# Performance work log

Measured on AMD Instinct MI355X. Metric: run time of the kernel, lower is better.

Reference implementation:

```python
import jax, jax.numpy as jnp
import numpy as np

LEAKY_SLOPE = 0.2  # PyG GATv2Conv default negative_slope


def gatv2_layer(x, src, dst, Wl, Wr, att, bias, concat):
    """PyG GATv2Conv (eval mode, dropout off, self-loops already in src/dst).
    x: [N, Din]; Wl/Wr: [Din, H*C]; att: [H, C]; bias: [H*C] or [C].
    """
    N = x.shape[0]
    H, C = att.shape
    xl = (x @ Wl).reshape(N, H, C)   # source transform
    xr = (x @ Wr).reshape(N, H, C)   # target transform
    # per-edge GATv2 score: att . leakyrelu(x_l[j] + x_r[i])
    e = jax.nn.leaky_relu(xl[src] + xr[dst], negative_slope=LEAKY_SLOPE)  # [E, H, C]
    score = jnp.einsum('ehc,hc->eh', e, att)                              # [E, H]
    # segment softmax over incoming edges of each dst node
    m = jax.ops.segment_max(score, dst, num_segments=N)                   # [N, H]
    a = jnp.exp(score - m[dst])
    denom = jax.ops.segment_sum(a, dst, num_segments=N)                   # [N, H]
    alpha = a / denom[dst]                                                # [E, H]
    out = jax.ops.segment_sum(xl[src] * alpha[..., None], dst, num_segments=N)  # [N, H, C]
    out = out.reshape(N, H * C) if concat else out.mean(axis=1)
    return out + bias


def setup_inputs() -> dict:
    key = jax.random.key(0)
    ks = jax.random.split(key, 10)
    N, D, E = 20000, 128, 320000
    HID, HEADS, OUT = 64, 8, 32
    x = jax.random.normal(ks[0], (N, D), dtype=jnp.float32)
    edge_index = jax.random.randint(ks[1], (2, E), 0, N)
    glorot = lambda k, shape, fan: jax.random.normal(k, shape, jnp.float32) * (1.0 / np.sqrt(fan))
    W1l = glorot(ks[2], (D, HEADS * HID), D)
    W1r = glorot(ks[3], (D, HEADS * HID), D)
    att1 = glorot(ks[4], (HEADS, HID), HID)
    b1 = jnp.zeros((HEADS * HID,), jnp.float32)
    W2l = glorot(ks[5], (HEADS * HID, 64), HEADS * HID)
    W2r = glorot(ks[6], (HEADS * HID, 64), HEADS * HID)
    att2 = glorot(ks[7], (1, 64), 64)
    b2 = jnp.zeros((64,), jnp.float32)
    Wlin = glorot(ks[8], (64, OUT), 64)
    blin = jnp.zeros((OUT,), jnp.float32)
    return {"x": x, "edge_index": edge_index, "W1l": W1l, "W1r": W1r, "att1": att1,
            "b1": b1, "W2l": W2l, "W2r": W2r, "att2": att2, "b2": b2,
            "Wlin": Wlin, "blin": blin}


def reference(x, edge_index, W1l, W1r, att1, b1, W2l, W2r, att2, b2, Wlin, blin):
    N = x.shape[0]
    loop = jnp.arange(N)
    src = jnp.concatenate([edge_index[0], loop])  # PyG add_self_loops=True
    dst = jnp.concatenate([edge_index[1], loop])
    h = jax.nn.elu(gatv2_layer(x, src, dst, W1l, W1r, att1, b1, concat=True))
    h = jax.nn.elu(gatv2_layer(h, src, dst, W2l, W2r, att2, b2, concat=False))
    return jax.nn.elu(h @ Wlin + blin)
```

## Files before the change

### kernel.cpp

```cpp
#include <hip/hip_runtime.h>
#include <hip/hip_bf16.h>

typedef __attribute__((ext_vector_type(8))) short short8;
typedef __attribute__((ext_vector_type(4))) short short4v;
typedef __attribute__((ext_vector_type(4))) float floatx4;
typedef __attribute__((ext_vector_type(2))) float float2v;
typedef __attribute__((ext_vector_type(4))) int int4v;
typedef __attribute__((ext_vector_type(2))) int int2v;

#define LOG2E 1.44269504f

__device__ __forceinline__ short f2b(float f) {
    __hip_bfloat16 hb = __float2bfloat16(f);
    unsigned short us; __builtin_memcpy(&us, &hb, 2);
    return (short)us;
}
__device__ __forceinline__ float2v bpair(int p) {
    unsigned ulo = ((unsigned)p) << 16;
    unsigned uhi = ((unsigned)p) & 0xFFFF0000u;
    float flo, fhi;
    __builtin_memcpy(&flo, &ulo, 4);
    __builtin_memcpy(&fhi, &uhi, 4);
    float2v r; r.x = flo; r.y = fhi; return r;
}

__device__ __forceinline__ float2v pk_add(float2v a, float2v b) {
    float2v d;
    asm("v_pk_add_f32 %0, %1, %2" : "=v"(d) : "v"(a), "v"(b));
    return d;
}
__device__ __forceinline__ float2v pk_fma(float2v a, float2v b, float2v c) {
    float2v d;
    asm("v_pk_fma_f32 %0, %1, %2, %3" : "=v"(d) : "v"(a), "v"(b), "v"(c));
    return d;
}
__device__ __forceinline__ float2v pk_abs(float2v a) {
    float2v d;
    d.x = __builtin_fabsf(a.x);
    d.y = __builtin_fabsf(a.y);
    return d;
}

template<int CTRL>
__device__ __forceinline__ float dppadd(float x) {
    int xi; __builtin_memcpy(&xi, &x, 4);
    int yi = __builtin_amdgcn_update_dpp(0, xi, CTRL, 0xF, 0xF, false);
    float y; __builtin_memcpy(&y, &yi, 4);
    return x + y;
}
__device__ __forceinline__ float red8(float x) {
    x = dppadd<0xB1>(x);
    x = dppadd<0x4E>(x);
    x = dppadd<0x141>(x);
    return x;
}
__device__ __forceinline__ float red16(float x) {
    return dppadd<0x140>(red8(x));
}

__global__ void prep_all(const float* __restrict__ x,
                         const float* __restrict__ W1l, const float* __restrict__ W1r,
                         const float* __restrict__ W2l, const float* __restrict__ W2r,
                         short* __restrict__ xb, short* __restrict__ w1t,
                         short* __restrict__ w2t, int nx4,
                         const int* __restrict__ esrc, const int* __restrict__ edst,
                         int E, int N, int* __restrict__ counts,
                         unsigned short* __restrict__ srcs) {
    int tid = blockIdx.x * blockDim.x + threadIdx.x;
    int ET = E + N;
    if (tid < ET) {
        int d, s;
        if (tid < E) { d = edst[tid]; s = esrc[tid]; }
        else { d = tid - E; s = d; }
        int pos = atomicAdd(&counts[d], 1);
        if (pos < 64) srcs[(d << 6) + pos] = (unsigned short)s;
    }
    int idx = tid;
    if (idx < nx4) {
        floatx4 v = *(const floatx4*)(x + idx * 4);
        short4v o; o[0] = f2b(v[0]); o[1] = f2b(v[1]); o[2] = f2b(v[2]); o[3] = f2b(v[3]);
        *(short4v*)(xb + idx * 4) = o;
        return;
    }
    idx -= nx4;
    if (idx < 131072) {
        int n = idx >> 7, k = idx & 127;
        float v = (n < 512) ? W1l[k * 512 + n] : W1r[k * 512 + (n - 512)];
        w1t[idx] = f2b(v);
        return;
    }
    idx -= 131072;
    if (idx < 65536) {
        int n = idx >> 9, k = idx & 511;
        float v = (n < 64) ? W2l[k * 64 + n] : W2r[k * 64 + (n - 64)];
        w2t[idx] = f2b(v);
    }
}

__global__ __launch_bounds__(256) void gemm1(const short* __restrict__ A,
                                             const short* __restrict__ Bt,
                                             short* __restrict__ xl1, short* __restrict__ xr1,
                                             int M) {
    __shared__ short As[64 * 136];
    __shared__ short Bs[128 * 136];
    int t = threadIdx.x;
    int w = t >> 6, L = t & 63, q = L >> 4, s = L & 15;
    int p = blockIdx.x + (blockIdx.y << 3);
    int my = gridDim.y;
    int ww = (p & 7) * my + (p >> 3);
    int M0 = (ww >> 3) * 64, N0 = (ww & 7) * 128;
    #pragma unroll
    for (int i = 0; i < 4; ++i) {
        int c = t + i * 256;
        int r = c >> 4, col = (c & 15) * 8;
        int gr = M0 + r;
        short8 v = {};
        if (gr < M) v = *(const short8*)(A + (size_t)gr * 128 + col);
        *(short8*)(&As[r * 136 + col]) = v;
    }
    #pragma unroll
    for (int i = 0; i < 8; ++i) {
        int c = t + i * 256;
        int r = c >> 4, col = (c & 15) * 8;
        short8 v = *(const short8*)(Bt + (size_t)(N0 + r) * 128 + col);
        *(short8*)(&Bs[r * 136 + col]) = v;
    }
    __syncthreads();
    short8 a[4];
    #pragma unroll
    for (int kk = 0; kk < 4; ++kk)
        a[kk] = *(const short8*)(&As[(w * 16 + s) * 136 + kk * 32 + q * 8]);
    floatx4 acc[8] = {};
    #pragma unroll
    for (int tt = 0; tt < 8; ++tt) {
        #pragma unroll
        for (int kk = 0; kk < 4; ++kk) {
            short8 b = *(const short8*)(&Bs[(tt * 16 + s) * 136 + kk * 32 + q * 8]);
            acc[tt] = __builtin_amdgcn_mfma_f32_16x16x32_bf16(a[kk], b, acc[tt], 0, 0, 0);
        }
    }
    __syncthreads();
    #pragma unroll
    for (int tt = 0; tt < 8; ++tt) {
        #pragma unroll
        for (int rg = 0; rg < 4; ++rg) {
            int rl = w * 16 + q * 4 + rg;
            As[rl * 136 + tt * 16 + s] = f2b(acc[tt][rg]);
        }
    }
    __syncthreads();
    short* Cb = (N0 < 512) ? xl1 : xr1;
    int cb = (N0 < 512) ? N0 : N0 - 512;
    size_t M64 = (size_t)M * 64;
    #pragma unroll
    for (int i = 0; i < 4; ++i) {
        int c = t + i * 256;
        int r = c >> 4, col = (c & 15) * 8;
        int row = M0 + r;
        if (row < M) {
            short8 v = *(const short8*)(&As[r * 136 + col]);
            int cc = cb + col;
            *(short8*)(Cb + (size_t)(cc >> 6) * M64 + (size_t)row * 64 + (cc & 63)) = v;
        }
    }
}

__global__ __launch_bounds__(256) void gemm2(const short* __restrict__ A,
                                             const short* __restrict__ Bt,
                                             short* __restrict__ C, int M) {
    __shared__ short As[32 * 72];
    __shared__ short Bs[64 * 72];
    int t = threadIdx.x;
    int w = t >> 6, L = t & 63, q = L >> 4, s = L & 15;
    int rw = (w >> 1) * 16, cw = (w & 1) * 32;
    int p = blockIdx.x + gridDim.x * blockIdx.y;
    int nwg = gridDim.x * 2;
    int qq = nwg >> 3, rr = nwg & 7;
    int kx = p & 7, tx = p >> 3;
    int ww = (kx < rr ? kx * (qq + 1) : rr * (qq + 1) + (kx - rr) * qq) + tx;
    int M0 = (ww >> 1) * 32, N0 = (ww & 1) * 64;
    size_t M64 = (size_t)M * 64;
    floatx4 acc[2] = {};
    for (int k0 = 0; k0 < 512; k0 += 64) {
        {
            int r = t >> 3, col = (t & 7) * 8;
            int gr = M0 + r;
            short8 v = {};
            if (gr < M) v = *(const short8*)(A + (size_t)(k0 >> 6) * M64 + (size_t)gr * 64 + col);
            *(short8*)(&As[r * 72 + col]) = v;
        }
        #pragma unroll
        for (int i = 0; i < 2; ++i) {
            int c = t + i * 256;
            int r = c >> 3, col = (c & 7) * 8;
            short8 v = *(const short8*)(Bt + (size_t)(N0 + r) * 512 + k0 + col);
            *(short8*)(&Bs[r * 72 + col]) = v;
        }
        __syncthreads();
        #pragma unroll
        for (int kk = 0; kk < 2; ++kk) {
            short8 a = *(const short8*)(&As[(rw + s) * 72 + kk * 32 + q * 8]);
            #pragma unroll
            for (int tt = 0; tt < 2; ++tt) {
                short8 b = *(const short8*)(&Bs[(cw + tt * 16 + s) * 72 + kk * 32 + q * 8]);
                acc[tt] = __builtin_amdgcn_mfma_f32_16x16x32_bf16(a, b, acc[tt], 0, 0, 0);
            }
        }
        __syncthreads();
    }
    #pragma unroll
    for (int tt = 0; tt < 2; ++tt) {
        #pragma unroll
        for (int rg = 0; rg < 4; ++rg) {
            int rl = rw + q * 4 + rg;
            As[rl * 72 + cw + tt * 16 + s] = f2b(acc[tt][rg]);
        }
    }
    __syncthreads();
    {
        int r = t >> 3, col = (t & 7) * 8;
        int row = M0 + r;
        if (row < M) {
            short8 v = *(const short8*)(&As[r * 72 + col]);
            *(short8*)(C + (size_t)row * 128 + N0 + col) = v;
        }
    }
}

__global__ __launch_bounds__(256) void gat_l1(const short* __restrict__ xlh,
                       const short* __restrict__ xrh,
                       const int* __restrict__ counts,
                       const unsigned short* __restrict__ srcs,
                       const float* __restrict__ att, const float* __restrict__ bias,
                       short* __restrict__ h1h, int Nn) {
    int bid = blockIdx.x;
    int h = bid & 7, nb = bid >> 3;
    int t = threadIdx.x;
    int w = t >> 6, L = t & 63;
    int i = nb * 4 + w;
    if (i >= Nn) return;
    int g = L >> 3;
    int o8 = (L & 7) * 8;
    size_t slice = (size_t)h * ((size_t)Nn * 64);
    const short* Bh = xlh + slice;
    float2v xrv[4], at6[4], at4[4];
    {
        float av[8];
        *(floatx4*)av       = *(const floatx4*)(att + h * 64 + o8);
        *(floatx4*)(av + 4) = *(const floatx4*)(att + h * 64 + o8 + 4);
        int4v x4 = *(const int4v*)(xrh + slice + (size_t)i * 64 + o8);
        #pragma unroll
        for (int c = 0; c < 4; ++c) {
            xrv[c] = bpair(x4[c]);
            at6[c].x = av[2 * c]     * (0.6f * LOG2E);
            at6[c].y = av[2 * c + 1] * (0.6f * LOG2E);
            at4[c].x = av[2 * c]     * (0.4f * LOG2E);
            at4[c].y = av[2 * c + 1] * (0.4f * LOG2E);
        }
    }
    int jv = srcs[(i << 6) + L];
    int deg = counts[i]; deg = deg > 64 ? 64 : deg;
    float2v acc[4] = {};
    float dnm = 0.f;

    auto fetchj = [&](int e) -> int {
        int idx = e + g;
        idx = idx < deg ? idx : 0;
        return __shfl(jv, idx, 64);
    };
    auto ldrow = [&](int j) -> int4v {
        return *(const int4v*)(Bh + (((unsigned)j) << 6) + o8);
    };
    auto process = [&](int4v a4, int e) {
        float2v v[4]; float2v pp = {};
        #pragma unroll
        for (int c = 0; c < 4; ++c) {
            v[c] = bpair(a4[c]);
            float2v tv = pk_add(v[c], xrv[c]);
            pp = pk_fma(at6[c], tv, pp);
            pp = pk_fma(at4[c], pk_abs(tv), pp);
        }
        float e2 = __builtin_amdgcn_exp2f(red8(pp.x + pp.y));
        e2 = (e + g < deg) ? e2 : 0.f;
        dnm += e2;
        float2v ev; ev.x = e2; ev.y = e2;
        #pragma unroll
        for (int c = 0; c < 4; ++c)
            acc[c] = pk_fma(ev, v[c], acc[c]);
    };

    int4v cur = ldrow(fetchj(0));
    int e = 0;
    for (; e + 8 < deg; e += 8) {
        int4v nxt = ldrow(fetchj(e + 8));
        process(cur, e);
        cur = nxt;
    }
    process(cur, e);

    dnm += __shfl_xor(dnm, 8, 64);
    dnm += __shfl_xor(dnm, 16, 64);
    dnm += __shfl_xor(dnm, 32, 64);
    #pragma unroll
    for (int c = 0; c < 4; ++c) {
        acc[c].x += __shfl_xor(acc[c].x, 8, 64);
        acc[c].x += __shfl_xor(acc[c].x, 16, 64);
        acc[c].x += __shfl_xor(acc[c].x, 32, 64);
        acc[c].y += __shfl_xor(acc[c].y, 8, 64);
        acc[c].y += __shfl_xor(acc[c].y, 16, 64);
        acc[c].y += __shfl_xor(acc[c].y, 32, 64);
    }
    if (g == 0) {
        float inv = 1.f / dnm;
        float bv[8];
        *(floatx4*)bv       = *(const floatx4*)(bias + h * 64 + o8);
        *(floatx4*)(bv + 4) = *(const floatx4*)(bias + h * 64 + o8 + 4);
        short8 ov;
        #pragma unroll
        for (int c = 0; c < 4; ++c) {
            float ox = fmaf(acc[c].x, inv, bv[2 * c]);
            float oy = fmaf(acc[c].y, inv, bv[2 * c + 1]);
            ox = ox > 0.f ? ox : __expf(ox) - 1.f;
            oy = oy > 0.f ? oy : __expf(oy) - 1.f;
            ov[2 * c] = f2b(ox);
            ov[2 * c + 1] = f2b(oy);
        }
        *(short8*)(h1h + slice + (size_t)i * 64 + o8) = ov;
    }
}

__global__ __launch_bounds__(256) void gat_l2_fin(const short* __restrict__ x2,
                        const int* __restrict__ counts,
                        const unsigned short* __restrict__ srcs,
                        const float* __restrict__ att, const float* __restrict__ bias,
                        const float* __restrict__ Wlin, const float* __restrict__ blin,
                        float* __restrict__ out, int Nn) {
    __shared__ float Ws[2048];
    __shared__ float bs[32];
    __shared__ float h2s[4][64];
    int t = threadIdx.x;
    for (int idx = t; idx < 2048; idx += 256) Ws[idx] = Wlin[idx];
    if (t < 32) bs[t] = blin[t];
    __syncthreads();
    int w = t >> 6, L = t & 63;
    int i = blockIdx.x * 4 + w;
    if (i >= Nn) return;
    int g = L >> 4;
    int lc = L & 15;
    int c4 = lc * 4;
    float2v xrv[2], at6[2], at4[2];
    {
        int2v xv = *(const int2v*)(x2 + (i << 7) + 64 + c4);
        xrv[0] = bpair(xv.x);
        xrv[1] = bpair(xv.y);
        floatx4 a4 = *(const floatx4*)(att + c4);
        at6[0].x = a4[0] * (0.6f * LOG2E); at6[0].y = a4[1] * (0.6f * LOG2E);
        at6[1].x = a4[2] * (0.6f * LOG2E); at6[1].y = a4[3] * (0.6f * LOG2E);
        at4[0].x = a4[0] * (0.4f * LOG2E); at4[0].y = a4[1] * (0.4f * LOG2E);
        at4[1].x = a4[2] * (0.4f * LOG2E); at4[1].y = a4[3] * (0.4f * LOG2E);
    }
    float dnm = 0.f;
    float2v acc0 = {}, acc1 = {};
    int kb = i << 6;
    int deg = counts[i]; deg = deg > 64 ? 64 : deg;
    int ke = kb + deg;
    const int2v* x2i = (const int2v*)x2;

    auto doedge = [&](int2v Vv, bool val) {
        float2v v0 = bpair(Vv.x), v1 = bpair(Vv.y);
        float2v t0 = pk_add(v0, xrv[0]), t1 = pk_add(v1, xrv[1]);
        float2v pp = pk_fma(at6[0], t0, at4[0] * pk_abs(t0));
        pp = pk_fma(at6[1], t1, pp);
        pp = pk_fma(at4[1], pk_abs(t1), pp);
        float e = val ? __builtin_amdgcn_exp2f(red16(pp.x + pp.y)) : 0.f;
        dnm += e;
        float2v e2; e2.x = e; e2.y = e;
        acc0 = pk_fma(e2, v0, acc0);
        acc1 = pk_fma(e2, v1, acc1);
    };

    for (int k0 = kb; k0 < ke; k0 += 16) {
        int ka = k0 + g, kc = k0 + 4 + g, kd = k0 + 8 + g, kf = k0 + 12 + g;
        bool va = ka < ke, vb = kc < ke, vc = kd < ke, vd = kf < ke;
        int ja = srcs[va ? ka : kb];
        int jb = srcs[vb ? kc : kb];
        int jc = srcs[vc ? kd : kb];
        int jd = srcs[vd ? kf : kb];
        int2v Va = x2i[(ja << 5) + lc];
        int2v Vb = x2i[(jb << 5) + lc];
        int2v Vc = x2i[(jc << 5) + lc];
        int2v Vd = x2i[(jd << 5) + lc];
        doedge(Va, va);
        doedge(Vb, vb);
        doedge(Vc, vc);
        doedge(Vd, vd);
    }
    #pragma unroll
    for (int m = 16; m <= 32; m <<= 1) {
        dnm += __shfl_xor(dnm, m, 64);
        acc0.x += __shfl_xor(acc0.x, m, 64);
        acc0.y += __shfl_xor(acc0.y, m, 64);
        acc1.x += __shfl_xor(acc1.x, m, 64);
        acc1.y += __shfl_xor(acc1.y, m, 64);
    }
    float inv = 1.f / dnm;
    floatx4 bv = *(const floatx4*)(bias + c4);
    float o0 = fmaf(acc0.x, inv, bv[0]);
    float o1 = fmaf(acc0.y, inv, bv[1]);
    float o2 = fmaf(acc1.x, inv, bv[2]);
    float o3 = fmaf(acc1.y, inv, bv[3]);
    o0 = o0 > 0.f ? o0 : __expf(o0) - 1.f;
    o1 = o1 > 0.f ? o1 : __expf(o1) - 1.f;
    o2 = o2 > 0.f ? o2 : __expf(o2) - 1.f;
    o3 = o3 > 0.f ? o3 : __expf(o3) - 1.f;
    if (L < 16) {
        floatx4 hv; hv[0] = o0; hv[1] = o1; hv[2] = o2; hv[3] = o3;
        *(floatx4*)(&h2s[w][c4]) = hv;
    }
    int oc = L & 31;
    float accl = 0.f;
    #pragma unroll
    for (int kk = 0; kk < 16; ++kk) {
        floatx4 hvv = *(const floatx4*)(&h2s[w][kk * 4]);
        accl = fmaf(hvv[0], Ws[(kk * 4 + 0) * 32 + oc], accl);
        accl = fmaf(hvv[1], Ws[(kk * 4 + 1) * 32 + oc], accl);
        accl = fmaf(hvv[2], Ws[(kk * 4 + 2) * 32 + oc], accl);
        accl = fmaf(hvv[3], Ws[(kk * 4 + 3) * 32 + oc], accl);
    }
    if (L < 32) {
        float r = accl + bs[oc];
        r = r > 0.f ? r : __expf(r) - 1.f;
        out[(size_t)i * 32 + oc] = r;
    }
}

extern "C" void kernel_launch(void* const* d_in, const int* in_sizes, int n_in,
                              void* d_out, int out_size, void* d_ws, size_t ws_size,
                              hipStream_t stream) {
    const float* x    = (const float*)d_in[0];
    const int*   ei   = (const int*)d_in[1];
    const float* W1l  = (const float*)d_in[2];
    const float* W1r  = (const float*)d_in[3];
    const float* att1 = (const float*)d_in[4];
    const float* b1   = (const float*)d_in[5];
    const float* W2l  = (const float*)d_in[6];
    const float* W2r  = (const float*)d_in[7];
    const float* att2 = (const float*)d_in[8];
    const float* b2   = (const float*)d_in[9];
    const float* Wlin = (const float*)d_in[10];
    const float* blin = (const float*)d_in[11];

    const int N  = in_sizes[0] / 128;
    const int E  = in_sizes[1] / 2;

    char* w = (char*)d_ws;
    size_t cur = 0;
    auto take = [&](size_t bytes) -> void* {
        void* p = w + cur;
        cur = (cur + bytes + 255) & ~(size_t)255;
        return p;
    };
    int*            counts = (int*)take((size_t)N * 4);
    unsigned short* srcs   = (unsigned short*)take((size_t)N * 64 * 2);
    short* xb     = (short*)take((size_t)N * 128 * 2);
    short* w1t    = (short*)take((size_t)1024 * 128 * 2);
    short* w2t    = (short*)take((size_t)128 * 512 * 2);
    short* xl1    = (short*)take((size_t)N * 512 * 2);
    short* xr1    = (short*)take((size_t)N * 512 * 2);
    short* h1     = (short*)take((size_t)N * 512 * 2);
    short* x2     = (short*)take((size_t)N * 128 * 2);

    hipMemsetAsync(counts, 0, (size_t)N * 4, stream);
    int nx4 = N * 32;
    int nconv = nx4 + 131072 + 65536;
    int nprep = (E + N) > nconv ? (E + N) : nconv;
    prep_all<<<(nprep + 255) / 256, 256, 0, stream>>>(x, W1l, W1r, W2l, W2r, xb, w1t, w2t,
                                                      nx4, ei, ei + E, E, N, counts, srcs);

    gemm1<<<dim3(8, (N + 63) / 64), 256, 0, stream>>>(xb, w1t, xl1, xr1, N);
    gat_l1<<<8 * ((N + 3) / 4), 256, 0, stream>>>(xl1, xr1, counts, srcs, att1, b1, h1, N);

    gemm2<<<dim3((N + 31) / 32, 2), 256, 0, stream>>>(h1, w2t, x2, N);
    gat_l2_fin<<<(N + 3) / 4, 256, 0, stream>>>(x2, counts, srcs, att2, b2, Wlin, blin,
                                                (float*)d_out, N);
}
```

Baseline: 217.2 us.

## Map one node per 8-lane group in GAT layer-1 aggregation, batch 8 row loads

The layer-1 attention kernel now gives each 8-lane group its own destination node, so a wavefront handles 8 nodes instead of one. This removes the cross-group shuffle reductions at the end. Each group loads 8 neighbor rows at once from source indices fetched with vector loads and lane shuffles, which raises memory-level parallelism. The trade-off is lane divergence: every group loops until the wave's maximum degree, and the grid is 8x smaller. The source index is masked to 15 bits, which assumes N fits in 32768.

```diff
diff --git a/kernel.cpp b/kernel.cpp
--- a/kernel.cpp
+++ b/kernel.cpp
@@ -237,93 +237,96 @@
     int h = bid & 7, nb = bid >> 3;
     int t = threadIdx.x;
     int w = t >> 6, L = t & 63;
-    int i = nb * 4 + w;
-    if (i >= Nn) return;
-    int g = L >> 3;
-    int o8 = (L & 7) * 8;
+    int u = L >> 3;
+    int c = L & 7;
+    int o8 = c * 8;
+    int i = (nb * 4 + w) * 8 + u;
+    bool inode = i < Nn;
+    int ic = inode ? i : 0;
     size_t slice = (size_t)h * ((size_t)Nn * 64);
-    const short* Bh = xlh + slice;
+    const char* Bp = (const char*)(xlh + slice);
+    int co = c << 4;
+
     float2v xrv[4], at6[4], at4[4];
     {
         float av[8];
         *(floatx4*)av       = *(const floatx4*)(att + h * 64 + o8);
         *(floatx4*)(av + 4) = *(const floatx4*)(att + h * 64 + o8 + 4);
-        int4v x4 = *(const int4v*)(xrh + slice + (size_t)i * 64 + o8);
-        #pragma unroll
-        for (int c = 0; c < 4; ++c) {
-            xrv[c] = bpair(x4[c]);
-            at6[c].x = av[2 * c]     * (0.6f * LOG2E);
-            at6[c].y = av[2 * c + 1] * (0.6f * LOG2E);
-            at4[c].x = av[2 * c]     * (0.4f * LOG2E);
-            at4[c].y = av[2 * c + 1] * (0.4f * LOG2E);
-        }
-    }
-    int jv = srcs[(i << 6) + L];
-    int deg = counts[i]; deg = deg > 64 ? 64 : deg;
+        int4v x4 = *(const int4v*)(xrh + slice + (size_t)ic * 64 + o8);
+        #pragma unroll
+        for (int k = 0; k < 4; ++k) {
+            xrv[k] = bpair(x4[k]);
+            at6[k].x = av[2 * k]     * (0.6f * LOG2E);
+            at6[k].y = av[2 * k + 1] * (0.6f * LOG2E);
+            at4[k].x = av[2 * k]     * (0.4f * LOG2E);
+            at4[k].y = av[2 * k + 1] * (0.4f * LOG2E);
+        }
+    }
+    int deg = counts[ic]; deg = deg > 64 ? 64 : deg;
+    if (!inode) deg = 0;
+    int degw = deg;
+    degw = max(degw, __shfl_xor(degw, 8, 64));
+    degw = max(degw, __shfl_xor(degw, 16, 64));
+    degw = max(degw, __shfl_xor(degw, 32, 64));
+
+    const unsigned short* sp = srcs + ((size_t)ic << 6);
+    int4v J = *(const int4v*)(sp + c * 8);
+    int ubase = L & 56;
+
     float2v acc[4] = {};
     float dnm = 0.f;
 
-    auto fetchj = [&](int e) -> int {
-        int idx = e + g;
-        idx = idx < deg ? idx : 0;
-        return __shfl(jv, idx, 64);
-    };
-    auto ldrow = [&](int j) -> int4v {
-        return *(const int4v*)(Bh + (((unsigned)j) << 6) + o8);
-    };
-    auto process = [&](int4v a4, int e) {
-        float2v v[4]; float2v pp = {};
-        #pragma unroll
-        for (int c = 0; c < 4; ++c) {
-            v[c] = bpair(a4[c]);
-            float2v tv = pk_add(v[c], xrv[c]);
-            pp = pk_fma(at6[c], tv, pp);
-            pp = pk_fma(at4[c], pk_abs(tv), pp);
-        }
-        float e2 = __builtin_amdgcn_exp2f(red8(pp.x + pp.y));
-        e2 = (e + g < deg) ? e2 : 0.f;
-        dnm += e2;
-        float2v ev; ev.x = e2; ev.y = e2;
-        #pragma unroll
-        for (int c = 0; c < 4; ++c)
-            acc[c] = pk_fma(ev, v[c], acc[c]);
-    };
-
-    int4v cur = ldrow(fetchj(0));
-    int e = 0;
-    for (; e + 8 < deg; e += 8) {
-        int4v nxt = ldrow(fetchj(e + 8));
-        process(cur, e);
-        cur = nxt;
-    }
-    process(cur, e);
-
-    dnm += __shfl_xor(dnm, 8, 64);
-    dnm += __shfl_xor(dnm, 16, 64);
-    dnm += __shfl_xor(dnm, 32, 64);
-    #pragma unroll
-    for (int c = 0; c < 4; ++c) {
-        acc[c].x += __shfl_xor(acc[c].x, 8, 64);
-        acc[c].x += __shfl_xor(acc[c].x, 16, 64);
-        acc[c].x += __shfl_xor(acc[c].x, 32, 64);
-        acc[c].y += __shfl_xor(acc[c].y, 8, 64);
-        acc[c].y += __shfl_xor(acc[c].y, 16, 64);
-        acc[c].y += __shfl_xor(acc[c].y, 32, 64);
-    }
-    if (g == 0) {
+    for (int ow = 0; ow < 8; ++ow) {
+        int s0 = ow << 3;
+        if (s0 >= degw) break;
+        int lane = ubase + ow;
+        int j01 = __shfl(J[0], lane, 64);
+        int j23 = __shfl(J[1], lane, 64);
+        int j45 = __shfl(J[2], lane, 64);
+        int j67 = __shfl(J[3], lane, 64);
+        int js[8];
+        js[0] = j01 & 0x7FFF; js[1] = (j01 >> 16) & 0x7FFF;
+        js[2] = j23 & 0x7FFF; js[3] = (j23 >> 16) & 0x7FFF;
+        js[4] = j45 & 0x7FFF; js[5] = (j45 >> 16) & 0x7FFF;
+        js[6] = j67 & 0x7FFF; js[7] = (j67 >> 16) & 0x7FFF;
+        int4v rows[8];
+        #pragma unroll
+        for (int k = 0; k < 8; ++k)
+            rows[k] = *(const int4v*)(Bp + (((unsigned)js[k] << 7) + co));
+        #pragma unroll
+        for (int k = 0; k < 8; ++k) {
+            float2v v[4]; float2v pp = {};
+            #pragma unroll
+            for (int q = 0; q < 4; ++q) {
+                v[q] = bpair(rows[k][q]);
+                float2v tv = pk_add(v[q], xrv[q]);
+                pp = pk_fma(at6[q], tv, pp);
+                pp = pk_fma(at4[q], pk_abs(tv), pp);
+            }
+            float e2 = __builtin_amdgcn_exp2f(red8(pp.x + pp.y));
+            e2 = (s0 + k < deg) ? e2 : 0.f;
+            dnm += e2;
+            float2v ev; ev.x = e2; ev.y = e2;
+            #pragma unroll
+            for (int q = 0; q < 4; ++q)
+                acc[q] = pk_fma(ev, v[q], acc[q]);
+        }
+    }
+
+    if (inode) {
         float inv = 1.f / dnm;
         float bv[8];
         *(floatx4*)bv       = *(const floatx4*)(bias + h * 64 + o8);
         *(floatx4*)(bv + 4) = *(const floatx4*)(bias + h * 64 + o8 + 4);
         short8 ov;
         #pragma unroll
-        for (int c = 0; c < 4; ++c) {
-            float ox = fmaf(acc[c].x, inv, bv[2 * c]);
-            float oy = fmaf(acc[c].y, inv, bv[2 * c + 1]);
+        for (int k = 0; k < 4; ++k) {
+            float ox = fmaf(acc[k].x, inv, bv[2 * k]);
+            float oy = fmaf(acc[k].y, inv, bv[2 * k + 1]);
             ox = ox > 0.f ? ox : __expf(ox) - 1.f;
             oy = oy > 0.f ? oy : __expf(oy) - 1.f;
-            ov[2 * c] = f2b(ox);
-            ov[2 * c + 1] = f2b(oy);
+            ov[2 * k] = f2b(ox);
+            ov[2 * k + 1] = f2b(oy);
         }
         *(short8*)(h1h + slice + (size_t)i * 64 + o8) = ov;
     }
@@ -478,7 +481,7 @@
                                                       nx4, ei, ei + E, E, N, counts, srcs);
 
     gemm1<<<dim3(8, (N + 63) / 64), 256, 0, stream>>>(xb, w1t, xl1, xr1, N);
-    gat_l1<<<8 * ((N + 3) / 4), 256, 0, stream>>>(xl1, xr1, counts, srcs, att1, b1, h1, N);
+    gat_l1<<<8 * ((N + 31) / 32), 256, 0, stream>>>(xl1, xr1, counts, srcs, att1, b1, h1, N);
 
     gemm2<<<dim3((N + 31) / 32, 2), 256, 0, stream>>>(h1, w2t, x2, N);
     gat_l2_fin<<<(N + 3) / 4, 256, 0, stream>>>(x2, counts, srcs, att2, b2, Wlin, blin,
```

Result: faster. 197.2 us, median of 2 (-9.2%).
